# Kernel tuning notes

Measured on AMD Instinct MI355X. Metric: run time of the kernel, lower is better.

The kernel has to match this reference:

```python
import jax, jax.numpy as jnp
import numpy as np

N_HEAD, D_MODEL, D_HEAD = 16, 1024, 64
EPS = 1e-5
SCALE = 1.0 / np.sqrt(D_HEAD)


def setup_inputs() -> dict:
    key = jax.random.key(0)
    k1, k2, k3 = jax.random.split(key, 3)
    slen, bsz = 2048, 4
    h = jax.random.normal(k1, (slen, bsz, D_MODEL), dtype=jnp.float32)
    w_qkvb = jax.random.normal(k2, (N_HEAD * (3 * D_HEAD + 1), D_MODEL), dtype=jnp.float32) / np.sqrt(D_MODEL)
    w_o = jax.random.normal(k3, (D_MODEL, N_HEAD * D_HEAD), dtype=jnp.float32) / np.sqrt(N_HEAD * D_HEAD)
    ln_g = jnp.ones((D_MODEL,), dtype=jnp.float32)
    ln_b = jnp.zeros((D_MODEL,), dtype=jnp.float32)
    return {"h": h, "w_qkvb": w_qkvb, "w_o": w_o, "ln_g": ln_g, "ln_b": ln_b}


def _layer_norm(x, g, b):
    mu = jnp.mean(x, axis=-1, keepdims=True)
    var = jnp.mean(jnp.square(x - mu), axis=-1, keepdims=True)
    return (x - mu) * jax.lax.rsqrt(var + EPS) * g + b


def _fast_weight_memory(q, k, v, beta):
    # q,k,v: [b,h,l,d]; beta: [b,h,l,1]. Delta-rule recurrence over l.
    b, hn, l, d = q.shape
    qs = jnp.moveaxis(q, 2, 0)      # [l,b,h,d]
    ks = jnp.moveaxis(k, 2, 0)
    vs = jnp.moveaxis(v, 2, 0)
    bs = jnp.moveaxis(beta, 2, 0)   # [l,b,h,1]

    def step(W, xs):
        qt, kt, vt, bt = xs
        v_old = jnp.einsum('bhij,bhj->bhi', W, kt)
        delta = bt * (vt - v_old)                     # [b,h,d]
        W = W + delta[..., :, None] * kt[..., None, :]
        out = jnp.einsum('bhij,bhj->bhi', W, qt)
        return W, out

    W0 = jnp.zeros((b, hn, d, d), dtype=q.dtype)
    _, outs = jax.lax.scan(step, W0, (qs, ks, vs, bs))
    return jnp.moveaxis(outs, 0, 2)  # [b,h,l,d]


def reference(h, w_qkvb, w_o, ln_g, ln_b):
    slen, bsz, _ = h.shape
    qkvb = (h @ w_qkvb.T).reshape(slen, bsz, N_HEAD, 3 * D_HEAD + 1)
    q, k, v, beta = jnp.split(qkvb, [D_HEAD, 2 * D_HEAD, 3 * D_HEAD], axis=-1)
    beta = jax.nn.sigmoid(beta)
    # -> [b, h, l, d]
    q = jnp.transpose(q, (1, 2, 0, 3))
    k = jnp.transpose(k, (1, 2, 0, 3))
    v = jnp.transpose(v, (1, 2, 0, 3))
    beta = jnp.transpose(beta, (1, 2, 0, 3))

    q = jax.nn.elu(q) + 1.0
    k = jax.nn.elu(k) + 1.0
    k = k / jnp.sum(k, axis=-1, keepdims=True)
    q = q / jnp.sum(q, axis=-1, keepdims=True)

    denom_acc = jnp.cumsum(k, axis=2)  # [b,h,l,d]
    # key denominator: <cumsum(k)[t-1], k_t>, with t=0 forced to 1
    shifted = jnp.concatenate(
        [jnp.zeros_like(denom_acc[:, :, :1]), denom_acc[:, :, :-1]], axis=2)
    key_denom = jnp.einsum('bhld,bhld->bhl', shifted, k)
    key_denom = jnp.concatenate(
        [jnp.ones_like(key_denom[:, :, :1]), key_denom[:, :, 1:]], axis=2)[..., None]
    beta = beta * key_denom
    k = k / (key_denom + EPS)

    denominator = jnp.einsum('bhld,bhld->bhl', denom_acc, q)[..., None]

    layer_out = _fast_weight_memory(q, k, v, beta)
    layer_out = SCALE * layer_out / (denominator + EPS)  # [b,h,l,d]

    layer_out = jnp.transpose(layer_out, (0, 2, 1, 3)).reshape(
        layer_out.shape[0], slen, N_HEAD * D_HEAD)
    layer_out = jnp.transpose(layer_out, (1, 0, 2))  # [l,b,h*d]

    attn_out = layer_out @ w_o.T
    return _layer_norm(h + attn_out, ln_g, ln_b)
```

## Files before the change

### kernel.cpp

```cpp
#include <hip/hip_runtime.h>
#include <cstdint>
#include <cstddef>

#define D_HEAD   64
#define NHEAD    16
#define DMODEL   1024
#define SLEN     2048
#define BSZ      4
#define MROWS    (SLEN*BSZ)
#define NQKVB    (NHEAD*(3*D_HEAD+1))
#define NQPAD    3200
#define EPSV     1e-5f
#define SCALEV   0.125f
#define CHK      64
#define NCH      (SLEN/CHK)

typedef short bf16x8 __attribute__((ext_vector_type(8)));
typedef float f32x4  __attribute__((ext_vector_type(4)));

__device__ __forceinline__ unsigned short f2bf(float f){
  unsigned int u = __float_as_uint(f);
  u = (u + 0x7fffu + ((u >> 16) & 1u)) >> 16;
  return (unsigned short)u;
}
__device__ __forceinline__ float bf2f(unsigned short s){
  return __uint_as_float(((unsigned int)s) << 16);
}

__device__ __forceinline__ void gload_lds16(const unsigned short* g, unsigned short* l){
  __builtin_amdgcn_global_load_lds((const __attribute__((address_space(1))) void*)g,
                                   (__attribute__((address_space(3))) void*)l, 16, 0, 0);
}

#define SWZ(row, col) ((col) ^ (((row)&7)<<3))

__global__ void cast_bf16_kernel(const float* __restrict__ src,
                                 unsigned short* __restrict__ dst, int n4){
  int stride = gridDim.x * blockDim.x;
  for (int i = blockIdx.x*blockDim.x + threadIdx.x; i < n4; i += stride){
    float4 f = ((const float4*)src)[i];
    ushort4 u;
    u.x = f2bf(f.x); u.y = f2bf(f.y); u.z = f2bf(f.z); u.w = f2bf(f.w);
    ((ushort4*)dst)[i] = u;
  }
}

template<bool OUT_BF16>
__global__ __launch_bounds__(256) void gemm_big_kernel(
    const unsigned short* __restrict__ A, const unsigned short* __restrict__ B,
    void* __restrict__ C, int M, int N, int K){
  __shared__ __align__(16) unsigned short sA[128*32];
  __shared__ __align__(16) unsigned short sB[128*32];
  int m0 = blockIdx.x * 128, n0 = blockIdx.y * 128;
  int tid = threadIdx.x;
  int wv = tid >> 6, ln = tid & 63;
  int lm = ln & 15, quad = ln >> 4;
  int wm = (wv >> 1) * 64, wn = (wv & 1) * 64;
  f32x4 acc[4][4] = {};

  for (int kt = 0; kt < K; kt += 32){
    __syncthreads();
    #pragma unroll
    for (int it = 0; it < 2; ++it){
      int s = wv*128 + it*64 + ln;
      int row = s >> 2, sg = s & 3;
      gload_lds16(A + (size_t)(m0+row)*K + kt + sg*8, sA + (size_t)(wv*128 + it*64)*8);
      gload_lds16(B + (size_t)(n0+row)*K + kt + sg*8, sB + (size_t)(wv*128 + it*64)*8);
    }
    __syncthreads();
    bf16x8 af[4], bfr[4];
    #pragma unroll
    for (int i = 0; i < 4; ++i){
      af[i]  = *(const bf16x8*)(sA + ((wm + i*16 + lm)*32 + quad*8));
      bfr[i] = *(const bf16x8*)(sB + ((wn + i*16 + lm)*32 + quad*8));
    }
    #pragma unroll
    for (int mi = 0; mi < 4; ++mi)
      #pragma unroll
      for (int ni = 0; ni < 4; ++ni)
        acc[mi][ni] = __builtin_amdgcn_mfma_f32_16x16x32_bf16(af[mi], bfr[ni], acc[mi][ni], 0, 0, 0);
  }

  #pragma unroll
  for (int mi = 0; mi < 4; ++mi){
    int rowm = m0 + wm + mi*16 + quad*4;
    #pragma unroll
    for (int ni = 0; ni < 4; ++ni){
      int col = n0 + wn + ni*16 + lm;
      size_t cb = (size_t)rowm * N + col;
      #pragma unroll
      for (int rr = 0; rr < 4; ++rr){
        float v = acc[mi][ni][rr];
        if (OUT_BF16) ((unsigned short*)C)[cb + (size_t)rr*N] = f2bf(v);
        else          ((float*)C)[cb + (size_t)rr*N] = v;
      }
    }
  }
}

__global__ __launch_bounds__(256) void prep_kernel(
    const unsigned short* __restrict__ qkvb,
    float* __restrict__ qb, float* __restrict__ kb,
    unsigned short* __restrict__ qb16, unsigned short* __restrict__ vb16,
    float4* __restrict__ scal){
  int gid = blockIdx.x*4 + (threadIdx.x >> 6);
  int ln  = threadIdx.x & 63;
  int m = gid >> 4, h = gid & 15;
  size_t rb = (size_t)m * NQPAD + (size_t)h * 193;
  float qr = bf2f(qkvb[rb + ln]);
  float kr = bf2f(qkvb[rb + 64 + ln]);
  float vr = bf2f(qkvb[rb + 128 + ln]);
  float br = bf2f(qkvb[rb + 192]);
  float q1 = qr > 0.f ? qr + 1.f : __expf(qr);
  float k1 = kr > 0.f ? kr + 1.f : __expf(kr);
  float sq = q1, sk = k1;
  #pragma unroll
  for (int off = 1; off < 64; off <<= 1){
    sq += __shfl_xor(sq, off, 64);
    sk += __shfl_xor(sk, off, 64);
  }
  float qn = q1 / sq, kn = k1 / sk;
  int b = m & 3, t = m >> 2;
  int bh = b*16 + h;
  size_t row = ((size_t)bh*SLEN + t)*64;
  qb[row + ln] = qn; kb[row + ln] = kn;
  qb16[row + SWZ(t, ln)] = f2bf(qn);
  vb16[row + ln] = f2bf(vr);
  if (ln == 0){
    float sb = 1.f / (1.f + __expf(-br));
    scal[(size_t)bh*SLEN + t] = make_float4(0.f, 0.f, 0.f, sb);
  }
}

#define NSEG 16
#define SEGL (SLEN/NSEG)
__global__ __launch_bounds__(64) void segsum_kernel(
    const float* __restrict__ kb, float* __restrict__ S){
  int bh = blockIdx.x, seg = blockIdx.y, ln = threadIdx.x;
  size_t base = ((size_t)bh*SLEN + (size_t)seg*SEGL)*64 + ln;
  float s = 0.f;
  #pragma unroll 4
  for (int t = 0; t < SEGL; ++t) s += kb[base + (size_t)t*64];
  S[((size_t)bh*NSEG + seg)*64 + ln] = s;
}
__global__ __launch_bounds__(64) void scan_kernel(
    const float* __restrict__ kb, const float* __restrict__ S,
    float* __restrict__ Ab){
  int bh = blockIdx.x, seg = blockIdx.y, ln = threadIdx.x;
  float acc = 0.f;
  for (int s = 0; s < seg; ++s) acc += S[((size_t)bh*NSEG + s)*64 + ln];
  size_t base = ((size_t)bh*SLEN + (size_t)seg*SEGL)*64 + ln;
  #pragma unroll 4
  for (int t = 0; t < SEGL; ++t){
    acc += kb[base + (size_t)t*64];
    Ab[base + (size_t)t*64] = acc;
  }
}

__global__ __launch_bounds__(256) void kden_kernel(
    const float* __restrict__ Ab, float* __restrict__ kb,
    const float* __restrict__ qb, unsigned short* __restrict__ kb16,
    float4* __restrict__ scal){
  int gid = blockIdx.x*4 + (threadIdx.x >> 6);
  int ln  = threadIdx.x & 63;
  int t = gid & (SLEN-1);
  size_t o = (size_t)gid*64 + ln;
  float a = Ab[o], kn = kb[o], qn = qb[o];
  float d0 = (a - kn)*kn, d1 = a*qn, d2 = kn*qn;
  #pragma unroll
  for (int off = 1; off < 64; off <<= 1){
    d0 += __shfl_xor(d0, off, 64);
    d1 += __shfl_xor(d1, off, 64);
    d2 += __shfl_xor(d2, off, 64);
  }
  float kd  = (t == 0) ? 1.f : d0;
  float inv = 1.f / (kd + EPSV);
  float kf = kn * inv;
  kb[o] = kf;
  kb16[(size_t)gid*64 + SWZ(t, ln)] = f2bf(kf);
  if (ln == 0){
    float4 s = scal[gid];
    scal[gid] = make_float4(s.w * kd, d2 * inv, SCALEV/(d1 + EPSV), 0.f);
  }
}

__global__ __launch_bounds__(64, 1) void precomp_kernel(
    const unsigned short* __restrict__ K16, const unsigned short* __restrict__ Q16,
    const float4* __restrict__ scal,
    unsigned short* __restrict__ Dg, unsigned short* __restrict__ Bg){
  __shared__ __align__(16) float sA[64*64];
  __shared__ float sbp[64];
  int inst = blockIdx.x;
  int bh = inst >> 5, ch = inst & 31;
  int ln = threadIdx.x, lm = ln & 15, quad = ln >> 4;
  const unsigned short* Kg = K16 + ((size_t)bh*SLEN + ch*CHK)*64;
  const unsigned short* Qg = Q16 + ((size_t)bh*SLEN + ch*CHK)*64;

  {
    f32x4 acc[4][4] = {};
    #pragma unroll
    for (int s = 0; s < 2; ++s){
      bf16x8 kf[4];
      #pragma unroll
      for (int i = 0; i < 4; ++i){
        int row = i*16+lm;
        kf[i] = *(const bf16x8*)(Kg + (size_t)row*64 + SWZ(row, s*32 + quad*8));
      }
      #pragma unroll
      for (int mi = 0; mi < 4; ++mi)
        #pragma unroll
        for (int ni = 0; ni < 4; ++ni)
          acc[mi][ni] = __builtin_amdgcn_mfma_f32_16x16x32_bf16(kf[mi], kf[ni], acc[mi][ni], 0, 0, 0);
    }
    #pragma unroll
    for (int mi = 0; mi < 4; ++mi)
      #pragma unroll
      for (int ni = 0; ni < 4; ++ni)
        #pragma unroll
        for (int rr = 0; rr < 4; ++rr)
          sA[(mi*16+quad*4+rr)*64 + ni*16+lm] = acc[mi][ni][rr];
  }
  sbp[ln] = scal[(size_t)bh*SLEN + ch*CHK + ln].x;
  __syncthreads();

  {
    f32x4 acc[4][4] = {};
    #pragma unroll
    for (int s = 0; s < 2; ++s){
      bf16x8 kf[4], qf[4];
      #pragma unroll
      for (int i = 0; i < 4; ++i){
        int row = i*16+lm;
        kf[i] = *(const bf16x8*)(Kg + (size_t)row*64 + SWZ(row, s*32 + quad*8));
        qf[i] = *(const bf16x8*)(Qg + (size_t)row*64 + SWZ(row, s*32 + quad*8));
      }
      #pragma unroll
      for (int mi = 0; mi < 4; ++mi)
        #pragma unroll
        for (int ni = 0; ni < 4; ++ni)
          acc[mi][ni] = __builtin_amdgcn_mfma_f32_16x16x32_bf16(qf[mi], kf[ni], acc[mi][ni], 0, 0, 0);
    }
    size_t io = (size_t)inst*4096;
    #pragma unroll
    for (int mi = 0; mi < 4; ++mi)
      #pragma unroll
      for (int ni = 0; ni < 4; ++ni)
        #pragma unroll
        for (int rr = 0; rr < 4; ++rr){
          int t = mi*16+quad*4+rr, j = ni*16+lm;
          float v = (j <= t) ? acc[mi][ni][rr] : 0.f;
          Bg[io + (size_t)t*64 + SWZ(t, j)] = f2bf(v);
        }
  }

  {
    float x[64];
    x[0] = (ln == 0) ? sbp[0] : 0.f;
    #pragma unroll
    for (int i = 1; i < 64; ++i){
      float bi = sbp[i];
      float s = 0.f;
      #pragma unroll
      for (int m4 = 0; m4*4 < i; ++m4){
        float4 a = *(const float4*)&sA[i*64 + m4*4];
        if (m4*4+0 < i) s += a.x * x[m4*4+0];
        if (m4*4+1 < i) s += a.y * x[m4*4+1];
        if (m4*4+2 < i) s += a.z * x[m4*4+2];
        if (m4*4+3 < i) s += a.w * x[m4*4+3];
      }
      x[i] = ((ln == i) ? bi : 0.f) - bi*s;
    }
    size_t io = (size_t)inst*4096;
    #pragma unroll
    for (int i = 0; i < 64; ++i)
      Dg[io + (size_t)i*64 + SWZ(i, ln)] = f2bf(x[i]);
  }
}

__global__ __launch_bounds__(256, 1) void chunk_kernel(
    const unsigned short* __restrict__ K16, const unsigned short* __restrict__ Q16,
    const unsigned short* __restrict__ V16,
    const unsigned short* __restrict__ Dg, const unsigned short* __restrict__ Bg,
    const float4* __restrict__ scal, unsigned short* __restrict__ lo){
  __shared__ __align__(16) unsigned short sK[4096];
  __shared__ __align__(16) unsigned short sQ[4096];
  __shared__ __align__(16) unsigned short sD[4096];
  __shared__ __align__(16) unsigned short sB[4096];
  __shared__ __align__(16) unsigned short sKT[4096];
  __shared__ __align__(16) unsigned short sV[1024];
  __shared__ __align__(16) unsigned short sX[1024];
  __shared__ __align__(16) unsigned short sDT[1024];
  __shared__ __align__(16) unsigned short sW[1024];
  int bh = blockIdx.x, rg = blockIdx.y;
  int tid = threadIdx.x, wv = tid >> 6, ln = tid & 63, lm = ln & 15, quad = ln >> 4;
  size_t sb = (size_t)bh*SLEN*64;
  const unsigned short* Kg = K16 + sb;
  const unsigned short* Qg = Q16 + sb;
  const unsigned short* Vg = V16 + sb;
  const float4* scp = scal + (size_t)bh*SLEN;
  size_t lobase = (size_t)(bh>>4)*DMODEL + (size_t)(bh&15)*64 + rg*16;

  auto dma8 = [&](const unsigned short* g, unsigned short* s){
    #pragma unroll
    for (int it = 0; it < 2; ++it)
      gload_lds16(g + (wv*2+it)*512 + ln*8, s + (wv*2+it)*512);
  };
  auto dma_chunk = [&](int ch){
    size_t co = (size_t)ch*CHK*64;
    dma8(Kg + co, sK);
    dma8(Qg + co, sQ);
    size_t io = ((size_t)bh*NCH + ch)*4096;
    dma8(Dg + io, sD);
    dma8(Bg + io, sB);
    if (wv == 0){
      gload_lds16(Vg + co + (size_t)(ln>>1)*64 + rg*16 + (ln&1)*8, sV);
      gload_lds16(Vg + co + (size_t)(32 + (ln>>1))*64 + rg*16 + (ln&1)*8, sV + 512);
    }
  };
  auto frag = [&](const unsigned short* S, int row, int kb)->bf16x8 {
    return *(const bf16x8*)(S + row*64 + SWZ(row, kb));
  };

  if (tid < 128) ((uint4*)sW)[tid] = make_uint4(0u,0u,0u,0u);
  f32x4 Wacc = {0,0,0,0};
  dma_chunk(0);

  for (int ch = 0; ch < NCH; ++ch){
    int tb = ch*CHK + wv*16 + quad*4;
    float sz0 = scp[tb+0].z, sz1 = scp[tb+1].z, sz2 = scp[tb+2].z, sz3 = scp[tb+3].z;
    __builtin_amdgcn_s_waitcnt(0x0F70);
    __syncthreads();

    f32x4 Macc = {0,0,0,0}, Mqacc = {0,0,0,0};
    #pragma unroll
    for (int s = 0; s < 2; ++s){
      int kb = s*32 + quad*8;
      bf16x8 ak = frag(sK, wv*16+lm, kb);
      bf16x8 aq = frag(sQ, wv*16+lm, kb);
      bf16x8 bw = frag(sW, lm, kb);
      Macc  = __builtin_amdgcn_mfma_f32_16x16x32_bf16(ak, bw, Macc, 0, 0, 0);
      Mqacc = __builtin_amdgcn_mfma_f32_16x16x32_bf16(aq, bw, Mqacc, 0, 0, 0);
    }
    int d0 = wv*16;
    uint4 kr0 = *(const uint4*)(sK + ln*64 + SWZ(ln, d0));
    uint4 kr1 = *(const uint4*)(sK + ln*64 + SWZ(ln, d0+8));
    #pragma unroll
    for (int rr = 0; rr < 4; ++rr){
      int t = wv*16 + quad*4 + rr;
      float x = bf2f(sV[t*16 + lm]) - Macc[rr];
      sX[lm*64 + SWZ(lm, t)] = f2bf(x);
    }
    {
      const unsigned short* k0p = (const unsigned short*)&kr0;
      const unsigned short* k1p = (const unsigned short*)&kr1;
      #pragma unroll
      for (int e = 0; e < 8; ++e){
        int d = d0 + e;
        sKT[d*64 + SWZ(d, ln)] = k0p[e];
      }
      #pragma unroll
      for (int e = 0; e < 8; ++e){
        int d = d0 + 8 + e;
        sKT[d*64 + SWZ(d, ln)] = k1p[e];
      }
    }
    __syncthreads();

    f32x4 Dacc = {0,0,0,0};
    #pragma unroll
    for (int s = 0; s < 2; ++s){
      int kb = s*32 + quad*8;
      bf16x8 ad = frag(sD, wv*16+lm, kb);
      bf16x8 bx = frag(sX, lm, kb);
      Dacc = __builtin_amdgcn_mfma_f32_16x16x32_bf16(ad, bx, Dacc, 0, 0, 0);
    }
    #pragma unroll
    for (int rr = 0; rr < 4; ++rr){
      int t = wv*16 + quad*4 + rr;
      sDT[lm*64 + SWZ(lm, t)] = f2bf(Dacc[rr]);
    }
    __syncthreads();

    f32x4 Oacc = Mqacc;
    #pragma unroll
    for (int s = 0; s < 2; ++s){
      int kb = s*32 + quad*8;
      bf16x8 ab = frag(sB, wv*16+lm, kb);
      bf16x8 bd = frag(sDT, lm, kb);
      Oacc = __builtin_amdgcn_mfma_f32_16x16x32_bf16(ab, bd, Oacc, 0, 0, 0);
      bf16x8 adt = frag(sDT, lm, kb);
      bf16x8 bkt = frag(sKT, wv*16+lm, kb);
      Wacc = __builtin_amdgcn_mfma_f32_16x16x32_bf16(adt, bkt, Wacc, 0, 0, 0);
    }
    #pragma unroll
    for (int rr = 0; rr < 4; ++rr){
      int tabs = ch*CHK + wv*16 + quad*4 + rr;
      float sz = (rr==0)?sz0:(rr==1)?sz1:(rr==2)?sz2:sz3;
      lo[lobase + (size_t)tabs*(BSZ*DMODEL) + lm] = f2bf(Oacc[rr] * sz);
    }
    __syncthreads();

    if (ch + 1 < NCH) dma_chunk(ch + 1);
    #pragma unroll
    for (int rr = 0; rr < 4; ++rr){
      int r = quad*4 + rr, d = wv*16 + lm;
      sW[r*64 + SWZ(r, d)] = f2bf(Wacc[rr]);
    }
  }
}

__global__ __launch_bounds__(256) void ln_kernel(
    const float* __restrict__ hin, const float* __restrict__ attn,
    const float* __restrict__ g, const float* __restrict__ bta,
    float* __restrict__ out){
  int row = blockIdx.x, tid = threadIdx.x;
  size_t rb = (size_t)row * DMODEL;
  float4 hv = ((const float4*)(hin + rb))[tid];
  float4 av = ((const float4*)(attn + rb))[tid];
  float4 x;
  x.x = hv.x + av.x; x.y = hv.y + av.y; x.z = hv.z + av.z; x.w = hv.w + av.w;
  float s  = x.x + x.y + x.z + x.w;
  float ss = x.x*x.x + x.y*x.y + x.z*x.z + x.w*x.w;
  #pragma unroll
  for (int off = 1; off < 64; off <<= 1){
    s  += __shfl_xor(s , off, 64);
    ss += __shfl_xor(ss, off, 64);
  }
  __shared__ float ls[4], lq[4];
  int wv = tid >> 6, ln = tid & 63;
  if (ln == 0){ ls[wv] = s; lq[wv] = ss; }
  __syncthreads();
  s  = ls[0] + ls[1] + ls[2] + ls[3];
  ss = lq[0] + lq[1] + lq[2] + lq[3];
  float mu  = s * (1.f/DMODEL);
  float var = ss * (1.f/DMODEL) - mu*mu;
  float rstd = rsqrtf(var + EPSV);
  float4 gv = ((const float4*)g)[tid], bv = ((const float4*)bta)[tid];
  float4 o;
  o.x = (x.x-mu)*rstd*gv.x + bv.x;
  o.y = (x.y-mu)*rstd*gv.y + bv.y;
  o.z = (x.z-mu)*rstd*gv.z + bv.z;
  o.w = (x.w-mu)*rstd*gv.w + bv.w;
  ((float4*)(out + rb))[tid] = o;
}

extern "C" void kernel_launch(void* const* d_in, const int* in_sizes, int n_in,
                              void* d_out, int out_size, void* d_ws, size_t ws_size,
                              hipStream_t stream){
  const float* h     = (const float*)d_in[0];
  const float* wqkvb = (const float*)d_in[1];
  const float* wo    = (const float*)d_in[2];
  const float* lng   = (const float*)d_in[3];
  const float* lnb   = (const float*)d_in[4];
  float* out = (float*)d_out;

  char* w = (char*)d_ws;
  auto take = [&](size_t bytes)->char*{
    char* p = w; w += (bytes + 255) & ~(size_t)255; return p;
  };
  unsigned short* h_bf    = (unsigned short*)take((size_t)MROWS*DMODEL*2);
  unsigned short* wq_bf   = (unsigned short*)take((size_t)NQPAD*DMODEL*2);
  unsigned short* wo_bf   = (unsigned short*)take((size_t)DMODEL*DMODEL*2);
  unsigned short* qkvb_bf = (unsigned short*)take((size_t)MROWS*NQPAD*2);
  float* qb   = (float*)take((size_t)MROWS*DMODEL*4 + 4096);
  float* kb   = (float*)take((size_t)MROWS*DMODEL*4 + 4096);
  float* Ab   = (float*)take((size_t)MROWS*DMODEL*4);
  float4* scal = (float4*)take((size_t)64*SLEN*16 + 4096);
  unsigned short* lo_bf = (unsigned short*)take((size_t)MROWS*DMODEL*2);
  float* Sseg = (float*)take((size_t)64*NSEG*64*4);
  unsigned short* kb16 = (unsigned short*)take((size_t)MROWS*DMODEL*2);
  unsigned short* qb16 = (unsigned short*)take((size_t)MROWS*DMODEL*2);
  unsigned short* vb16 = (unsigned short*)take((size_t)MROWS*DMODEL*2);
  unsigned short* Dg = (unsigned short*)Ab;
  unsigned short* Bg = (unsigned short*)Ab + (size_t)64*NCH*4096;
  float* attn = Ab;

  cast_bf16_kernel<<<2048, 256, 0, stream>>>(h,     h_bf,  MROWS*DMODEL/4);
  cast_bf16_kernel<<<1024, 256, 0, stream>>>(wqkvb, wq_bf, NQKVB*DMODEL/4);
  cast_bf16_kernel<<<512,  256, 0, stream>>>(wo,    wo_bf, DMODEL*DMODEL/4);

  gemm_big_kernel<true><<<dim3(MROWS/128, NQPAD/128), 256, 0, stream>>>(
      h_bf, wq_bf, qkvb_bf, MROWS, NQPAD, DMODEL);

  prep_kernel<<<MROWS*NHEAD/4, 256, 0, stream>>>(qkvb_bf, qb, kb, qb16, vb16, scal);
  segsum_kernel<<<dim3(64, NSEG), 64, 0, stream>>>(kb, Sseg);
  scan_kernel<<<dim3(64, NSEG), 64, 0, stream>>>(kb, Sseg, Ab);
  kden_kernel<<<64*SLEN/4, 256, 0, stream>>>(Ab, kb, qb, kb16, scal);
  precomp_kernel<<<64*NCH, 64, 0, stream>>>(kb16, qb16, scal, Dg, Bg);
  chunk_kernel<<<dim3(64, 4), 256, 0, stream>>>(kb16, qb16, vb16, Dg, Bg, scal, lo_bf);

  gemm_big_kernel<false><<<dim3(MROWS/128, DMODEL/128), 256, 0, stream>>>(
      lo_bf, wo_bf, attn, MROWS, DMODEL, DMODEL);

  ln_kernel<<<MROWS, 256, 0, stream>>>(h, attn, lng, lnb, out);
  (void)in_sizes; (void)n_in; (void)out_size; (void)ws_size;
}
```

Baseline: 403.8 us.

## Replace GEMM with 256x256 tiled, double-buffered 8-wave pipelined MFMA kernel

Replaces the simple 128x128 single-buffered GEMM with a 256x256-tile, 512-thread kernel. It uses double-buffered swizzled LDS, interleaves global-to-LDS loads with MFMA phases under explicit waitcnt and barriers, and remaps workgroups for better L2 locality. NQPAD grows to 3328 so N divides by 256, at the cost of extra padded columns. The aim is to hide memory latency and cut LDS bank conflicts in the two projection GEMMs. The trade-offs are high register pressure, 128KB of LDS per block, and fragile hand-tuned synchronisation.

```diff
diff --git a/kernel.cpp b/kernel.cpp
--- a/kernel.cpp
+++ b/kernel.cpp
@@ -9,7 +9,7 @@
 #define BSZ      4
 #define MROWS    (SLEN*BSZ)
 #define NQKVB    (NHEAD*(3*D_HEAD+1))
-#define NQPAD    3200
+#define NQPAD    3328
 #define EPSV     1e-5f
 #define SCALEV   0.125f
 #define CHK      64
@@ -45,48 +45,126 @@
   }
 }
 
+#define GBAR  do{ asm volatile("" ::: "memory"); __builtin_amdgcn_s_barrier(); asm volatile("" ::: "memory"); }while(0)
+#define WVM2  asm volatile("s_waitcnt vmcnt(2)" ::: "memory")
+#define WLG0  asm volatile("s_waitcnt lgkmcnt(0)" ::: "memory")
+#define WLG8  asm volatile("s_waitcnt lgkmcnt(8)" ::: "memory")
+
+#define LDA(sb_, mih_) do{ \
+  _Pragma("unroll") \
+  for (int m2 = 0; m2 < 4; ++m2) \
+    _Pragma("unroll") \
+    for (int ks = 0; ks < 2; ++ks) \
+      aF[m2][ks] = frag(sb_, wmi*128 + (mih_)*64 + m2*16 + lm, ks); \
+}while(0)
+
+#define LDB(sb_, nih_) do{ \
+  _Pragma("unroll") \
+  for (int n2 = 0; n2 < 2; ++n2) \
+    _Pragma("unroll") \
+    for (int ks = 0; ks < 2; ++ks) \
+      bF[(nih_)*2+n2][ks] = frag(sb_, wni*64 + (nih_)*32 + n2*16 + lm, ks); \
+}while(0)
+
+#define MMA(mih_, nih_) do{ \
+  __builtin_amdgcn_s_setprio(1); \
+  _Pragma("unroll") \
+  for (int m2 = 0; m2 < 4; ++m2) \
+    _Pragma("unroll") \
+    for (int n2 = 0; n2 < 2; ++n2) \
+      _Pragma("unroll") \
+      for (int ks = 0; ks < 2; ++ks) \
+        acc[(mih_)*4+m2][(nih_)*2+n2] = __builtin_amdgcn_mfma_f32_16x16x32_bf16( \
+            aF[m2][ks], bF[(nih_)*2+n2][ks], acc[(mih_)*4+m2][(nih_)*2+n2], 0, 0, 0); \
+  __builtin_amdgcn_s_setprio(0); \
+}while(0)
+
 template<bool OUT_BF16>
-__global__ __launch_bounds__(256) void gemm_big_kernel(
+__global__ __launch_bounds__(512, 2) void gemm8p_kernel(
     const unsigned short* __restrict__ A, const unsigned short* __restrict__ B,
-    void* __restrict__ C, int M, int N, int K){
-  __shared__ __align__(16) unsigned short sA[128*32];
-  __shared__ __align__(16) unsigned short sB[128*32];
-  int m0 = blockIdx.x * 128, n0 = blockIdx.y * 128;
+    void* __restrict__ C, int M, int N, int K, int tm){
+  __shared__ __align__(16) unsigned short sA[2][256*64];
+  __shared__ __align__(16) unsigned short sB[2][256*64];
   int tid = threadIdx.x;
-  int wv = tid >> 6, ln = tid & 63;
-  int lm = ln & 15, quad = ln >> 4;
-  int wm = (wv >> 1) * 64, wn = (wv & 1) * 64;
-  f32x4 acc[4][4] = {};
-
-  for (int kt = 0; kt < K; kt += 32){
-    __syncthreads();
-    #pragma unroll
-    for (int it = 0; it < 2; ++it){
-      int s = wv*128 + it*64 + ln;
-      int row = s >> 2, sg = s & 3;
-      gload_lds16(A + (size_t)(m0+row)*K + kt + sg*8, sA + (size_t)(wv*128 + it*64)*8);
-      gload_lds16(B + (size_t)(n0+row)*K + kt + sg*8, sB + (size_t)(wv*128 + it*64)*8);
-    }
-    __syncthreads();
-    bf16x8 af[4], bfr[4];
-    #pragma unroll
-    for (int i = 0; i < 4; ++i){
-      af[i]  = *(const bf16x8*)(sA + ((wm + i*16 + lm)*32 + quad*8));
-      bfr[i] = *(const bf16x8*)(sB + ((wn + i*16 + lm)*32 + quad*8));
-    }
-    #pragma unroll
-    for (int mi = 0; mi < 4; ++mi)
-      #pragma unroll
-      for (int ni = 0; ni < 4; ++ni)
-        acc[mi][ni] = __builtin_amdgcn_mfma_f32_16x16x32_bf16(af[mi], bfr[ni], acc[mi][ni], 0, 0, 0);
-  }
+  int wv = tid >> 6, ln = tid & 63, lm = ln & 15, quad = ln >> 4;
+  int nwg = gridDim.x, wg = blockIdx.x;
+  int cpx = nwg >> 3;
+  int swzb = (wg & 7)*cpx + (wg >> 3);
+  int bm = swzb % tm, bn = swzb / tm;
+  int m0 = bm << 8, n0 = bn << 8;
+  int wmi = wv >> 2, wni = wv & 3;
+  const unsigned short* Ag = A + (size_t)m0*K;
+  const unsigned short* Bg = B + (size_t)n0*K;
+
+  f32x4 acc[8][4] = {};
+  bf16x8 aF[4][2], bF[4][2];
+
+  int e0 = wv*64 + ln;
+  int r0row = e0 >> 3, r0cb = e0 & 7;
+  int e1 = 512 + e0;
+  int r1row = e1 >> 3, r1cb = e1 & 7;
+  size_t gsrc0 = (size_t)r0row*K + ((r0cb ^ (r0row & 7)) << 3);
+  size_t gsrc1 = (size_t)r1row*K + ((r1cb ^ (r1row & 7)) << 3);
+  int ldst0 = (wv*64) * 8;
+  int ldst1 = (512 + wv*64) * 8;
+
+  auto stage = [&](const unsigned short* g, unsigned short* sb, int h, int kt){
+    gload_lds16(g + (size_t)h*128*K + kt + gsrc0, sb + h*8192 + ldst0);
+    gload_lds16(g + (size_t)h*128*K + kt + gsrc1, sb + h*8192 + ldst1);
+  };
+  auto frag = [&](const unsigned short* sb, int row, int ks)->bf16x8 {
+    return *(const bf16x8*)(sb + row*64 + ((((ks<<2)+quad) ^ (row & 7)) << 3));
+  };
+
+  stage(Ag, sA[0], 0, 0);
+  stage(Ag, sA[0], 1, 0);
+  stage(Bg, sB[0], 0, 0);
+  stage(Bg, sB[0], 1, 0);
+  stage(Ag, sA[1], 0, 64);
+  WVM2;
+  GBAR;
+
+  int nit = K >> 7;
+  for (int i = 0; i < nit; ++i){
+    int k1 = (i<<7) + 64;
+    int k2 = ((i<<7) + 128) & (K-1);
+    int k3 = ((i<<7) + 192) & (K-1);
+
+    LDA(sA[0], 0); LDB(sB[0], 0);
+    stage(Ag, sA[1], 1, k1);
+    WLG8;
+    GBAR; WLG0; MMA(0,0); GBAR;
+    LDB(sB[0], 1);
+    stage(Bg, sB[1], 0, k1);
+    GBAR; WLG0; MMA(0,1); GBAR;
+    LDA(sA[0], 1);
+    stage(Bg, sB[1], 1, k1);
+    GBAR; WLG0; MMA(1,0); GBAR;
+    stage(Ag, sA[0], 0, k2);
+    WVM2;
+    GBAR; MMA(1,1); GBAR;
+    LDA(sA[1], 0); LDB(sB[1], 0);
+    stage(Ag, sA[0], 1, k2);
+    WLG8;
+    GBAR; WLG0; MMA(0,0); GBAR;
+    LDB(sB[1], 1);
+    stage(Bg, sB[0], 0, k2);
+    GBAR; WLG0; MMA(0,1); GBAR;
+    LDA(sA[1], 1);
+    stage(Bg, sB[0], 1, k2);
+    GBAR; WLG0; MMA(1,0); GBAR;
+    stage(Ag, sA[1], 0, k3);
+    WVM2;
+    GBAR; MMA(1,1); GBAR;
+  }
+  asm volatile("s_waitcnt vmcnt(0)" ::: "memory");
 
   #pragma unroll
-  for (int mi = 0; mi < 4; ++mi){
-    int rowm = m0 + wm + mi*16 + quad*4;
+  for (int mi = 0; mi < 8; ++mi){
+    int rowm = m0 + wmi*128 + mi*16 + quad*4;
     #pragma unroll
     for (int ni = 0; ni < 4; ++ni){
-      int col = n0 + wn + ni*16 + lm;
+      int col = n0 + wni*64 + ni*16 + lm;
       size_t cb = (size_t)rowm * N + col;
       #pragma unroll
       for (int rr = 0; rr < 4; ++rr){
@@ -96,7 +174,16 @@
       }
     }
   }
-}
+  (void)M;
+}
+
+#undef LDA
+#undef LDB
+#undef MMA
+#undef GBAR
+#undef WVM2
+#undef WLG0
+#undef WLG8
 
 __global__ __launch_bounds__(256) void prep_kernel(
     const unsigned short* __restrict__ qkvb,
@@ -479,8 +566,8 @@
   cast_bf16_kernel<<<1024, 256, 0, stream>>>(wqkvb, wq_bf, NQKVB*DMODEL/4);
   cast_bf16_kernel<<<512,  256, 0, stream>>>(wo,    wo_bf, DMODEL*DMODEL/4);
 
-  gemm_big_kernel<true><<<dim3(MROWS/128, NQPAD/128), 256, 0, stream>>>(
-      h_bf, wq_bf, qkvb_bf, MROWS, NQPAD, DMODEL);
+  gemm8p_kernel<true><<<(MROWS/256)*(NQPAD/256), 512, 0, stream>>>(
+      h_bf, wq_bf, qkvb_bf, MROWS, NQPAD, DMODEL, MROWS/256);
 
   prep_kernel<<<MROWS*NHEAD/4, 256, 0, stream>>>(qkvb_bf, qb, kb, qb16, vb16, scal);
   segsum_kernel<<<dim3(64, NSEG), 64, 0, stream>>>(kb, Sseg);
@@ -489,8 +576,8 @@
   precomp_kernel<<<64*NCH, 64, 0, stream>>>(kb16, qb16, scal, Dg, Bg);
   chunk_kernel<<<dim3(64, 4), 256, 0, stream>>>(kb16, qb16, vb16, Dg, Bg, scal, lo_bf);
 
-  gemm_big_kernel<false><<<dim3(MROWS/128, DMODEL/128), 256, 0, stream>>>(
-      lo_bf, wo_bf, attn, MROWS, DMODEL, DMODEL);
+  gemm8p_kernel<false><<<(MROWS/256)*(DMODEL/256), 512, 0, stream>>>(
+      lo_bf, wo_bf, attn, MROWS, DMODEL, DMODEL, MROWS/256);
 
   ln_kernel<<<MROWS, 256, 0, stream>>>(h, attn, lng, lnb, out);
   (void)in_sizes; (void)n_in; (void)out_size; (void)ws_size;
```

After: 395.9 us. 1.02x faster.
